# Performance work log

Hardware: AMD Instinct MI355X
Metric: run time of the kernel (lower is better)

## Reference

```python
import jax, jax.numpy as jnp
import numpy as np
from jax import lax

DILATION = 2


def setup_inputs() -> dict:
    key = jax.random.key(0)
    k1, k2, k3 = jax.random.split(key, 3)
    x = jax.random.normal(k1, (2048, 4096), dtype=jnp.float32)      # [T, num_inputs]
    weights = jax.random.normal(k2, (32, 16), dtype=jnp.float32)    # [num_lags, num_filters]
    biases = jax.random.normal(k3, (16,), dtype=jnp.float32) * 0.1  # [num_filters]
    return {"x": x, "weights": weights, "biases": biases}


def reference(x, weights, biases):
    T, num_inputs = x.shape
    L, F = weights.shape  # num_lags, num_filters

    # pos_constraint: clip weights at 0; normalize_weights: l2-normalize over lag axis
    w_p = jnp.maximum(weights, 0.0)
    w_pn = w_p * lax.rsqrt(jnp.maximum(jnp.sum(w_p * w_p, axis=0, keepdims=True), 1e-12))

    # reverse in time, pad num_lags zeros at the end -> causal filter of length 2L
    padded_filt = jnp.concatenate([w_pn[::-1], jnp.zeros((L, F), dtype=w_pn.dtype)], axis=0)
    kernel = padded_filt.reshape(2 * L, 1, 1, F)  # HWIO

    # [T, num_inputs] -> transpose -> [num_inputs, T, 1, 1] (NHWC, batch = input units)
    shaped_input = x.T.reshape(num_inputs, T, 1, 1)

    pre = lax.conv_general_dilated(
        shaped_input, kernel,
        window_strides=(1, 1),
        padding='SAME',
        rhs_dilation=(DILATION, 1),
        dimension_numbers=('NHWC', 'HWIO', 'NHWC'),
    )  # [num_inputs, T, 1, F]

    post = jax.nn.relu(pre + biases)  # bias broadcast over filters, relu activation

    # transpose to [T, num_inputs, 1, F] -> [T, num_inputs*F]
    out = jnp.transpose(post, (1, 0, 2, 3)).reshape(T, num_inputs * F)
    return out
```

## Files before the change

kernel.cpp:

```cpp
#include <hip/hip_runtime.h>


constexpr int T = 2048;
constexpr int N = 4096;
constexpr int L = 32;
constexpr int F = 16;
constexpr int NC = 128;
constexpr int NCHUNK = N / NC;
constexpr int NR = 33;
constexpr int OUT_STRIDE = N * F;

typedef float f4 __attribute__((ext_vector_type(4)));
typedef float f2 __attribute__((ext_vector_type(2)));

__global__ __launch_bounds__(256, 2)
void tlayer_kernel(const float* __restrict__ x,
                   const float* __restrict__ w,
                   const float* __restrict__ bias,
                   float* __restrict__ out)
{
    __shared__ __align__(16) float xs[2][NR * NC];
    __shared__ float sw[L * F];
    __shared__ float sscale[F];

    const int tid = threadIdx.x;
    const int b   = blockIdx.x;
    const int t0  = (b & 1) + (b >> 1) * 4;
    const int tb  = t0 + 2;

    sw[tid]       = fmaxf(w[tid], 0.f);
    sw[tid + 256] = fmaxf(w[tid + 256], 0.f);
    __syncthreads();
    if (tid < F) {
        float s = 0.f;
        #pragma unroll
        for (int l = 0; l < L; ++l) { float v = sw[l * F + tid]; s += v * v; }
        sscale[tid] = rsqrtf(fmaxf(s, 1e-12f));
    }
    __syncthreads();
    sw[tid]       *= sscale[tid & 15];
    sw[tid + 256] *= sscale[tid & 15];
    __syncthreads();

    const int fp = tid & 7;
    const int ng = tid >> 3;

    f2 wr[L];
    #pragma unroll
    for (int l = 0; l < L; ++l)
        wr[l] = *(const f2*)(sw + l * F + fp * 2);
    const f2 b2 = *(const f2*)(bias + fp * 2);


    {
        #pragma unroll
        for (int u = 0; u < 4; ++u) {
            const int idx = tid + u * 256;
            const int r = idx >> 5, c4 = idx & 31;
            const int g = tb - 1 - 2 * r;
            f4 v = {0.f, 0.f, 0.f, 0.f};
            if (g >= 0) v = *(const f4*)(x + (size_t)g * N + c4 * 4);
            *(f4*)(&xs[0][r * NC + c4 * 4]) = v;
        }
        if (tid < 32) {
            const int g = tb - 65;
            f4 v = {0.f, 0.f, 0.f, 0.f};
            if (g >= 0) v = *(const f4*)(x + (size_t)g * N + tid * 4);
            *(f4*)(&xs[0][32 * NC + tid * 4]) = v;
        }
    }
    __syncthreads();

    float* orowA = out + (size_t)t0 * OUT_STRIDE;
    float* orowB = out + (size_t)tb * OUT_STRIDE;

    #pragma unroll 1
    for (int c = 0; c < NCHUNK; ++c) {
        const int cur = c & 1;

        f4 ld[5];
        if (c + 1 < NCHUNK) {
            const int cn1 = (c + 1) * NC;
            #pragma unroll
            for (int u = 0; u < 4; ++u) {
                const int idx = tid + u * 256;
                const int r = idx >> 5, c4 = idx & 31;
                const int g = tb - 1 - 2 * r;
                ld[u] = {0.f, 0.f, 0.f, 0.f};
                if (g >= 0) ld[u] = *(const f4*)(x + (size_t)g * N + cn1 + c4 * 4);
            }
            ld[4] = {0.f, 0.f, 0.f, 0.f};
            if (tid < 32) {
                const int g = tb - 65;
                if (g >= 0) ld[4] = *(const f4*)(x + (size_t)g * N + cn1 + tid * 4);
            }
        }

        const float* xb = &xs[cur][4 * ng];
        f2 aA[4] = {b2, b2, b2, b2};
        f2 aB[4] = {b2, b2, b2, b2};
        #pragma unroll
        for (int r = 0; r < NR; ++r) {
            const f4 xv = *(const f4*)(xb + r * NC);
            if (r < L) {
                const f2 wl = wr[r];
                aB[0] += wl * xv[0]; aB[1] += wl * xv[1];
                aB[2] += wl * xv[2]; aB[3] += wl * xv[3];
            }
            if (r >= 1) {
                const f2 wl = wr[r - 1];
                aA[0] += wl * xv[0]; aA[1] += wl * xv[1];
                aA[2] += wl * xv[2]; aA[3] += wl * xv[3];
            }
        }

        const int nbase = c * NC + 4 * ng;
        #pragma unroll
        for (int k = 0; k < 4; ++k) {
            f2 rA, rB;
            rA[0] = fmaxf(aA[k][0], 0.f); rA[1] = fmaxf(aA[k][1], 0.f);
            rB[0] = fmaxf(aB[k][0], 0.f); rB[1] = fmaxf(aB[k][1], 0.f);
            *(f2*)(orowA + (size_t)(nbase + k) * F + fp * 2) = rA;
            *(f2*)(orowB + (size_t)(nbase + k) * F + fp * 2) = rB;
        }

        if (c + 1 < NCHUNK) {
            #pragma unroll
            for (int u = 0; u < 4; ++u) {
                const int idx = tid + u * 256;
                const int r = idx >> 5, c4 = idx & 31;
                *(f4*)(&xs[cur ^ 1][r * NC + c4 * 4]) = ld[u];
            }
            if (tid < 32)
                *(f4*)(&xs[cur ^ 1][32 * NC + tid * 4]) = ld[4];
        }
        __syncthreads();
    }
}

extern "C" void kernel_launch(void* const* d_in, const int* in_sizes, int n_in,
                              void* d_out, int out_size, void* d_ws, size_t ws_size,
                              hipStream_t stream) {
    const float* x    = (const float*)d_in[0];
    const float* w    = (const float*)d_in[1];
    const float* bias = (const float*)d_in[2];
    float* out = (float*)d_out;

    dim3 grid(T / 2);
    tlayer_kernel<<<grid, 256, 0, stream>>>(x, w, bias, out);
}
```

Baseline: 616.4 us.

## Compute eight same-parity time outputs per block to reuse staged input rows

Each block now computes 8 output time steps of one parity, spaced by the dilation, instead of 2. It stages 39 rows of x per chunk instead of 33, so each loaded input row feeds up to 8 output accumulators. The aim is less redundant global-to-LDS input traffic per output. The grid drops to 256 blocks with occupancy 1, and the 64 accumulator floats per thread raise register pressure. Output writes, which dominate traffic, are unchanged.

Measured after the change: 607.4 us. Within noise of the previous version (-1.5%).

```diff
diff --git a/kernel.cpp b/kernel.cpp
--- a/kernel.cpp
+++ b/kernel.cpp
@@ -5,15 +5,16 @@
 constexpr int N = 4096;
 constexpr int L = 32;
 constexpr int F = 16;
+constexpr int KT = 8;
 constexpr int NC = 128;
 constexpr int NCHUNK = N / NC;
-constexpr int NR = 33;
+constexpr int NR = 39;
 constexpr int OUT_STRIDE = N * F;
 
 typedef float f4 __attribute__((ext_vector_type(4)));
 typedef float f2 __attribute__((ext_vector_type(2)));
 
-__global__ __launch_bounds__(256, 2)
+__global__ __launch_bounds__(256, 1)
 void tlayer_kernel(const float* __restrict__ x,
                    const float* __restrict__ w,
                    const float* __restrict__ bias,
@@ -24,9 +25,8 @@
     __shared__ float sscale[F];
 
     const int tid = threadIdx.x;
-    const int b   = blockIdx.x;
-    const int t0  = (b & 1) + (b >> 1) * 4;
-    const int tb  = t0 + 2;
+    const int g   = blockIdx.x;
+    const int t0  = (g & 1) + (g >> 1) * 16;
 
     sw[tid]       = fmaxf(w[tid], 0.f);
     sw[tid + 256] = fmaxf(w[tid + 256], 0.f);
@@ -40,16 +40,6 @@
     __syncthreads();
     sw[tid]       *= sscale[tid & 15];
     sw[tid + 256] *= sscale[tid & 15];
-    __syncthreads();
-
-    const int fp = tid & 7;
-    const int ng = tid >> 3;
-
-    f2 wr[L];
-    #pragma unroll
-    for (int l = 0; l < L; ++l)
-        wr[l] = *(const f2*)(sw + l * F + fp * 2);
-    const f2 b2 = *(const f2*)(bias + fp * 2);
 
 
     {
@@ -57,22 +47,30 @@
         for (int u = 0; u < 4; ++u) {
             const int idx = tid + u * 256;
             const int r = idx >> 5, c4 = idx & 31;
-            const int g = tb - 1 - 2 * r;
+            const int gr = t0 - 63 + 2 * r;
             f4 v = {0.f, 0.f, 0.f, 0.f};
-            if (g >= 0) v = *(const f4*)(x + (size_t)g * N + c4 * 4);
+            if (gr >= 0) v = *(const f4*)(x + (size_t)gr * N + c4 * 4);
             *(f4*)(&xs[0][r * NC + c4 * 4]) = v;
         }
-        if (tid < 32) {
-            const int g = tb - 65;
+        if (tid < 224) {
+            const int idx = tid + 1024;
+            const int r = idx >> 5, c4 = idx & 31;
+            const int gr = t0 - 63 + 2 * r;
             f4 v = {0.f, 0.f, 0.f, 0.f};
-            if (g >= 0) v = *(const f4*)(x + (size_t)g * N + tid * 4);
-            *(f4*)(&xs[0][32 * NC + tid * 4]) = v;
+            if (gr >= 0) v = *(const f4*)(x + (size_t)gr * N + c4 * 4);
+            *(f4*)(&xs[0][r * NC + c4 * 4]) = v;
         }
     }
     __syncthreads();
 
-    float* orowA = out + (size_t)t0 * OUT_STRIDE;
-    float* orowB = out + (size_t)tb * OUT_STRIDE;
+    const int fp  = tid & 7;
+    const int nl4 = tid >> 3;
+
+    f2 wr[L];
+    #pragma unroll
+    for (int l = 0; l < L; ++l)
+        wr[l] = *(const f2*)(sw + l * F + fp * 2);
+    const f2 b2 = *(const f2*)(bias + fp * 2);
 
     #pragma unroll 1
     for (int c = 0; c < NCHUNK; ++c) {
@@ -85,43 +83,51 @@
             for (int u = 0; u < 4; ++u) {
                 const int idx = tid + u * 256;
                 const int r = idx >> 5, c4 = idx & 31;
-                const int g = tb - 1 - 2 * r;
+                const int gr = t0 - 63 + 2 * r;
                 ld[u] = {0.f, 0.f, 0.f, 0.f};
-                if (g >= 0) ld[u] = *(const f4*)(x + (size_t)g * N + cn1 + c4 * 4);
+                if (gr >= 0) ld[u] = *(const f4*)(x + (size_t)gr * N + cn1 + c4 * 4);
             }
             ld[4] = {0.f, 0.f, 0.f, 0.f};
-            if (tid < 32) {
-                const int g = tb - 65;
-                if (g >= 0) ld[4] = *(const f4*)(x + (size_t)g * N + cn1 + tid * 4);
+            if (tid < 224) {
+                const int idx = tid + 1024;
+                const int r = idx >> 5, c4 = idx & 31;
+                const int gr = t0 - 63 + 2 * r;
+                if (gr >= 0) ld[4] = *(const f4*)(x + (size_t)gr * N + cn1 + c4 * 4);
             }
         }
 
-        const float* xb = &xs[cur][4 * ng];
-        f2 aA[4] = {b2, b2, b2, b2};
-        f2 aB[4] = {b2, b2, b2, b2};
+        f2 acc[KT][4];
+        #pragma unroll
+        for (int i = 0; i < KT; ++i)
+            #pragma unroll
+            for (int k = 0; k < 4; ++k) acc[i][k] = b2;
+
         #pragma unroll
         for (int r = 0; r < NR; ++r) {
-            const f4 xv = *(const f4*)(xb + r * NC);
-            if (r < L) {
-                const f2 wl = wr[r];
-                aB[0] += wl * xv[0]; aB[1] += wl * xv[1];
-                aB[2] += wl * xv[2]; aB[3] += wl * xv[3];
-            }
-            if (r >= 1) {
-                const f2 wl = wr[r - 1];
-                aA[0] += wl * xv[0]; aA[1] += wl * xv[1];
-                aA[2] += wl * xv[2]; aA[3] += wl * xv[3];
+            const f4 xv = *(const f4*)(&xs[cur][r * NC + nl4 * 4]);
+            #pragma unroll
+            for (int i = 0; i < KT; ++i) {
+                if (r >= i && r <= 31 + i) {
+                    const f2 wl = wr[31 + i - r];
+                    acc[i][0] += wl * xv[0];
+                    acc[i][1] += wl * xv[1];
+                    acc[i][2] += wl * xv[2];
+                    acc[i][3] += wl * xv[3];
+                }
             }
         }
 
-        const int nbase = c * NC + 4 * ng;
+        const int cb = c * NC + nl4 * 4;
         #pragma unroll
-        for (int k = 0; k < 4; ++k) {
-            f2 rA, rB;
-            rA[0] = fmaxf(aA[k][0], 0.f); rA[1] = fmaxf(aA[k][1], 0.f);
-            rB[0] = fmaxf(aB[k][0], 0.f); rB[1] = fmaxf(aB[k][1], 0.f);
-            *(f2*)(orowA + (size_t)(nbase + k) * F + fp * 2) = rA;
-            *(f2*)(orowB + (size_t)(nbase + k) * F + fp * 2) = rB;
+        for (int i = 0; i < KT; ++i) {
+            float* orow = out + (size_t)(t0 + 2 * i) * OUT_STRIDE + fp * 2;
+            #pragma unroll
+            for (int k = 0; k < 4; ++k) {
+                f2 v;
+                v[0] = fmaxf(acc[i][k][0], 0.f);
+                v[1] = fmaxf(acc[i][k][1], 0.f);
+                *(f2*)(orow + (size_t)(cb + k) * F) = v;
+            }
         }
 
         if (c + 1 < NCHUNK) {
@@ -131,8 +137,11 @@
                 const int r = idx >> 5, c4 = idx & 31;
                 *(f4*)(&xs[cur ^ 1][r * NC + c4 * 4]) = ld[u];
             }
-            if (tid < 32)
-                *(f4*)(&xs[cur ^ 1][32 * NC + tid * 4]) = ld[4];
+            if (tid < 224) {
+                const int idx = tid + 1024;
+                const int r = idx >> 5, c4 = idx & 31;
+                *(f4*)(&xs[cur ^ 1][r * NC + c4 * 4]) = ld[4];
+            }
         }
         __syncthreads();
     }
@@ -146,6 +155,6 @@
     const float* bias = (const float*)d_in[2];
     float* out = (float*)d_out;
 
-    dim3 grid(T / 2);
+    dim3 grid(256);
     tlayer_kernel<<<grid, 256, 0, stream>>>(x, w, bias, out);
 }
```
